# Kernel optimization log

Measured on AMD Instinct MI355X. Metric: run time of the kernel, lower is better.

## Reference

```python
import jax, jax.numpy as jnp
import numpy as np

N = 100000
INPLANES = 256
WIDTH = 104          # floor(256 * 26 / 64)
SCALE = 4
NUMS = SCALE - 1     # 3 branch convs
K = 27               # 3^3 kernel offsets for 3D kernel_size=3
EPS = 1e-5


def setup_inputs() -> dict:
    key = jax.random.key(0)
    ks = jax.random.split(key, 12)
    x_feat = jax.random.normal(ks[0], (N, INPLANES), dtype=jnp.float32)
    # neighbor map: index N means "no neighbor" (padded zero row)
    nbr_idx = jax.random.randint(ks[1], (N, K), 0, N + 1)
    ws = WIDTH * SCALE
    W1 = jax.random.normal(ks[2], (INPLANES, ws), dtype=jnp.float32) * (1.0 / np.sqrt(INPLANES))
    g1 = jnp.ones((ws,), jnp.float32)
    b1 = jnp.zeros((ws,), jnp.float32)
    Wc = jax.random.normal(ks[3], (NUMS, K, WIDTH, WIDTH), dtype=jnp.float32) * (1.0 / np.sqrt(K * WIDTH))
    gc = jnp.ones((NUMS, WIDTH), jnp.float32)
    bc = jnp.zeros((NUMS, WIDTH), jnp.float32)
    W3 = jax.random.normal(ks[4], (ws, INPLANES), dtype=jnp.float32) * (1.0 / np.sqrt(ws))
    g3 = jnp.ones((INPLANES,), jnp.float32)
    b3 = jnp.zeros((INPLANES,), jnp.float32)
    return {"x_feat": x_feat, "nbr_idx": nbr_idx, "W1": W1, "g1": g1, "b1": b1,
            "Wc": Wc, "gc": gc, "bc": bc, "W3": W3, "g3": g3, "b3": b3}


def _bn(x, g, b):
    # training-mode batch norm over the point dimension
    m = jnp.mean(x, axis=0)
    v = jnp.var(x, axis=0)
    return (x - m) * jax.lax.rsqrt(v + EPS) * g + b


def _sparse_conv(feat, nbr_idx, Wk):
    # gather-GEMM-scatter sparse conv: out[n] = sum_k feat[nbr[n,k]] @ Wk[k]
    # index == N hits the appended zero row (missing neighbor)
    fp = jnp.concatenate([feat, jnp.zeros((1, feat.shape[1]), feat.dtype)], axis=0)
    out = jnp.zeros((feat.shape[0], Wk.shape[2]), feat.dtype)
    for k in range(Wk.shape[0]):  # fixed small set of 27 kernel offsets
        out = out + fp[nbr_idx[:, k]] @ Wk[k]
    return out


def reference(x_feat, nbr_idx, W1, g1, b1, Wc, gc, bc, W3, g3, b3):
    out = jax.nn.relu(_bn(x_feat @ W1, g1, b1))          # [N, width*scale]
    spx = [out[:, i * WIDTH:(i + 1) * WIDTH] for i in range(SCALE)]
    parts = []
    sp = None
    for i in range(NUMS):
        # stype='normal', same coord map -> features_at_coordinates is identity
        sp_in = spx[i] if i == 0 else sp + spx[i]
        sp = jax.nn.relu(_bn(_sparse_conv(sp_in, nbr_idx, Wc[i]), gc[i], bc[i]))
        parts.append(sp)
    parts.append(spx[SCALE - 1])                          # scale != 1, normal
    cat = jnp.concatenate(parts, axis=1)                  # [N, width*scale]
    out = _bn(cat @ W3, g3, b3) + x_feat                  # residual (no downsample)
    return jax.nn.relu(out)
```

## Files before the change

### kernel.cpp

```cpp
#include <hip/hip_runtime.h>

#define NPTS 100000
#define INC 256
#define WID 104
#define WSC 416
#define KOFF 27
#define EPSV 1e-5f

typedef unsigned short u16;
typedef float f32x4 __attribute__((ext_vector_type(4)));
typedef short s16x8 __attribute__((ext_vector_type(8)));

__device__ __forceinline__ u16 f2bf(float f) {
  unsigned u = __builtin_bit_cast(unsigned, f);
  u += 0x7FFFu + ((u >> 16) & 1u);
  return (u16)(u >> 16);
}
__device__ __forceinline__ float bf2f(u16 h) {
  unsigned u = ((unsigned)h) << 16;
  return __builtin_bit_cast(float, u);
}
__device__ __forceinline__ void mfma16(f32x4& d, s16x8 a, s16x8 b) {
  asm("v_mfma_f32_16x16x32_bf16 %0, %1, %2, %0" : "+v"(d) : "v"(a), "v"(b));
}
__device__ __forceinline__ void rawbar() {
  __builtin_amdgcn_s_barrier();
  __builtin_amdgcn_sched_barrier(0);
}

#define ST1_OFF 0
#define STC0_OFF 7488
#define STC1_OFF 9360
#define STC2_OFF 11232
#define ST3_OFF 13104
#define ST_TOTAL 17712

#define SPAD 128

__global__ __launch_bounds__(256) void k_prep_w1w3(const float* __restrict__ w1,
    const float* __restrict__ w3, u16* __restrict__ w1t, u16* __restrict__ w3t) {
  int i = blockIdx.x * 256 + threadIdx.x;
  if (i < 416 * 256) {
    int n = i >> 8, k = i & 255;
    w1t[i] = f2bf(w1[(size_t)k * WSC + n]);
  } else if (i < 2 * 416 * 256) {
    int o = i - 416 * 256;
    int n = o / WSC, k = o - n * WSC;
    w3t[o] = f2bf(w3[(size_t)k * INC + n]);
  }
}

__global__ __launch_bounds__(256) void k_prep_wc(const float* __restrict__ wc,
                                                 u16* __restrict__ wct) {
  __shared__ float w[WID * WID];
  int b = blockIdx.x, t = threadIdx.x;
  const float* s = wc + (size_t)b * WID * WID;
  for (int i = t; i < WID * WID; i += 256) w[i] = s[i];
  __syncthreads();
  u16* d = wct + (size_t)b * 112 * WID;
  for (int o = t; o < 112 * WID; o += 256) {
    int n = o / WID, kin = o - n * WID;
    d[o] = f2bf((n < WID) ? w[kin * WID + n] : 0.f);
  }
}

__global__ void k_init(float* __restrict__ st, u16* __restrict__ spxp) {
  const s16x8 hz = {0, 0, 0, 0, 0, 0, 0, 0};
  int i = blockIdx.x * 256 + threadIdx.x;
  if (i < ST_TOTAL) st[i] = 0.f;
  for (int task = i; task < (NPTS + 1) * 3; task += gridDim.x * 256) {
    int r = task / 3, c = task - 3 * r;
    *(s16x8*)(spxp + (size_t)r * SPAD + (13 + c) * 8) = hz;
  }
  if (blockIdx.x == 0 && threadIdx.x < 13)
    *(s16x8*)(spxp + (size_t)NPTS * SPAD + threadIdx.x * 8) = hz;
}

__global__ __launch_bounds__(256) void k_xbf(const float* __restrict__ x,
                                             u16* __restrict__ xb) {
  const int total = NPTS * INC / 8;
  for (int i = blockIdx.x * 256 + threadIdx.x; i < total; i += gridDim.x * 256) {
    const f32x4* s = (const f32x4*)(x + (size_t)i * 8);
    f32x4 v0 = s[0], v1 = s[1];
    s16x8 h;
#pragma unroll
    for (int j = 0; j < 4; ++j) { h[j] = (short)f2bf(v0[j]); h[4 + j] = (short)f2bf(v1[j]); }
    *(s16x8*)(xb + (size_t)i * 8) = h;
  }
}

__global__ __launch_bounds__(256) void k_gemm1(const u16* __restrict__ xb,
    const u16* __restrict__ w1t, u16* __restrict__ y1, float* __restrict__ stats) {
  __shared__ char Al[128 * 128];
  __shared__ char Bl[112 * 128];
  const int t = threadIdx.x, rowbase = blockIdx.x * 128, cb = blockIdx.y;
  const int lane = t & 63, wv = t >> 6, lr = lane & 15, lg = lane >> 4;
  const f32x4 fz = {0.f, 0.f, 0.f, 0.f};
  const s16x8 hz = {0, 0, 0, 0, 0, 0, 0, 0};
  f32x4 acc[2][7];
#pragma unroll
  for (int i = 0; i < 2; ++i)
#pragma unroll
    for (int j = 0; j < 7; ++j) acc[i][j] = fz;
  s16x8 pa[4], pb[4];

  auto issue = [&](int st) {
#pragma unroll
    for (int it = 0; it < 4; ++it) {
      int task = t + it * 256, r = task >> 3, c = task & 7, gr = rowbase + r;
      pa[it] = hz;
      if (gr < NPTS) pa[it] = *(const s16x8*)(xb + (size_t)gr * INC + st * 64 + c * 8);
      pb[it] = hz;
      if (task < 832)
        pb[it] = *(const s16x8*)(w1t + (size_t)(cb * WID + r) * INC + st * 64 + c * 8);
    }
  };
  auto writeT = [&]() {
#pragma unroll
    for (int it = 0; it < 4; ++it) {
      int task = t + it * 256, r = task >> 3, c = task & 7;
      *(s16x8*)(Al + ((r * 128 + c * 16) ^ ((r & 7) << 4))) = pa[it];
      if (task < 896) *(s16x8*)(Bl + ((r * 128 + c * 16) ^ ((r & 7) << 4))) = pb[it];
    }
  };
  auto compute = [&]() {
#pragma unroll
    for (int kc = 0; kc < 2; ++kc) {
      int co = kc * 64 + lg * 16;
      s16x8 a[2], b[7];
#pragma unroll
      for (int mt = 0; mt < 2; ++mt) {
        int r = wv * 32 + mt * 16 + lr;
        a[mt] = *(const s16x8*)(Al + ((r * 128 + co) ^ ((r & 7) << 4)));
      }
#pragma unroll
      for (int ct = 0; ct < 7; ++ct) {
        int r = ct * 16 + lr;
        b[ct] = *(const s16x8*)(Bl + ((r * 128 + co) ^ ((r & 7) << 4)));
      }
#pragma unroll
      for (int mt = 0; mt < 2; ++mt)
#pragma unroll
        for (int ct = 0; ct < 7; ++ct) mfma16(acc[mt][ct], a[mt], b[ct]);
    }
  };

  issue(0);
  for (int st = 0; st < 4; ++st) {
    writeT();
    __syncthreads();
    if (st < 3) issue(st + 1);
    compute();
    if (st < 3) rawbar();
  }
  __syncthreads();
  float* S = (float*)Al;
#pragma unroll
  for (int ct = 0; ct < 7; ++ct) {
    float s = 0.f, q = 0.f;
#pragma unroll
    for (int mt = 0; mt < 2; ++mt)
#pragma unroll
      for (int j = 0; j < 4; ++j) { float v = acc[mt][ct][j]; s += v; q += v * v; }
    s += __shfl_xor(s, 16); s += __shfl_xor(s, 32);
    q += __shfl_xor(q, 16); q += __shfl_xor(q, 32);
    if (lane < 16) {
      S[wv * 224 + ct * 16 + lane] = s;
      S[wv * 224 + 112 + ct * 16 + lane] = q;
    }
  }
  __syncthreads();
  if (t < 224) {
    float v = S[t] + S[224 + t] + S[448 + t] + S[672 + t];
    int cl = (t < 112) ? t : t - 112;
    if (cl < WID) {
      float* base = stats + (blockIdx.x & 7) * 832;
      atomicAdd(base + ((t < 112) ? 0 : WSC) + cb * WID + cl, v);
    }
  }
  __syncthreads();
#pragma unroll
  for (int mt = 0; mt < 2; ++mt)
#pragma unroll
    for (int ct = 0; ct < 7; ++ct)
#pragma unroll
      for (int j = 0; j < 4; ++j) {
        int r = rowbase + wv * 32 + mt * 16 + lg * 4 + j;
        int cl = ct * 16 + lr;
        if (r < NPTS && cl < WID)
          y1[(size_t)r * WSC + cb * WID + cl] = f2bf(acc[mt][ct][j]);
      }
}

__global__ __launch_bounds__(256) void k_conv(const u16* __restrict__ src,
    const int* __restrict__ nbr, const u16* __restrict__ wct,
    u16* __restrict__ z, float* __restrict__ stats) {
  __shared__ char Al[128 * 208];
  __shared__ char Bl[112 * 208];
  const int t = threadIdx.x, rowbase = blockIdx.x * 128;
  const int lane = t & 63, wv = t >> 6, lr = lane & 15, lg = lane >> 4;
  const f32x4 fz = {0.f, 0.f, 0.f, 0.f};
  const s16x8 hz = {0, 0, 0, 0, 0, 0, 0, 0};
  f32x4 acc[2][7];
#pragma unroll
  for (int i = 0; i < 2; ++i)
#pragma unroll
    for (int j = 0; j < 7; ++j) acc[i][j] = fz;
  s16x8 pa[8], pb[6];
  int pidx[8];

  auto idxIssue = [&](int kk) {
#pragma unroll
    for (int it = 0; it < 8; ++it) {
      int r = (t + it * 256) >> 4, gr = rowbase + r;
      pidx[it] = (gr < NPTS) ? nbr[gr * KOFF + kk] : NPTS;
    }
  };
  auto gatherIssue = [&]() {
#pragma unroll
    for (int it = 0; it < 8; ++it) {
      int c = (t + it * 256) & 15;
      pa[it] = hz;
      if (c < 13)
        pa[it] = *(const s16x8*)(src + (size_t)pidx[it] * SPAD + c * 8);
    }
  };
  auto loadB = [&](int k) {
#pragma unroll
    for (int it = 0; it < 6; ++it) {
      int task = t + it * 256;
      if (task < 1456) {
        int r = task / 13, c = task - 13 * r;
        pb[it] = *(const s16x8*)(wct + ((size_t)k * 112 + r) * WID + c * 8);
      }
    }
  };
  auto writeA = [&]() {
#pragma unroll
    for (int it = 0; it < 8; ++it) {
      int task = t + it * 256, r = task >> 4, c = task & 15;
      if (c < 13) *(s16x8*)(Al + r * 208 + c * 16) = pa[it];
    }
  };
  auto writeB = [&]() {
#pragma unroll
    for (int it = 0; it < 6; ++it) {
      int task = t + it * 256;
      if (task < 1456) {
        int r = task / 13, c = task - 13 * r;
        *(s16x8*)(Bl + r * 208 + c * 16) = pb[it];
      }
    }
  };
  auto compute = [&]() {
#pragma unroll
    for (int kc = 0; kc < 3; ++kc) {
      int co = kc * 64 + lg * 16;
      s16x8 a[2], b[7];
#pragma unroll
      for (int mt = 0; mt < 2; ++mt)
        a[mt] = *(const s16x8*)(Al + (wv * 32 + mt * 16 + lr) * 208 + co);
#pragma unroll
      for (int ct = 0; ct < 7; ++ct)
        b[ct] = *(const s16x8*)(Bl + (ct * 16 + lr) * 208 + co);
#pragma unroll
      for (int mt = 0; mt < 2; ++mt)
#pragma unroll
        for (int ct = 0; ct < 7; ++ct) mfma16(acc[mt][ct], a[mt], b[ct]);
    }
    {
      s16x8 a[2], b[7];
#pragma unroll
      for (int mt = 0; mt < 2; ++mt)
        a[mt] = (lg == 0) ? *(const s16x8*)(Al + (wv * 32 + mt * 16 + lr) * 208 + 192) : hz;
#pragma unroll
      for (int ct = 0; ct < 7; ++ct)
        b[ct] = (lg == 0) ? *(const s16x8*)(Bl + (ct * 16 + lr) * 208 + 192) : hz;
#pragma unroll
      for (int mt = 0; mt < 2; ++mt)
#pragma unroll
        for (int ct = 0; ct < 7; ++ct) mfma16(acc[mt][ct], a[mt], b[ct]);
    }
  };

  idxIssue(0);
  gatherIssue();
  loadB(0);
  idxIssue(1);
  for (int k = 0; k < KOFF; ++k) {
    writeA();
    writeB();
    __syncthreads();
    if (k < KOFF - 1) {
      gatherIssue();
      loadB(k + 1);
      if (k < KOFF - 2) idxIssue(k + 2);
    }
    compute();
    if (k < KOFF - 1) rawbar();
  }
  __syncthreads();
  float* S = (float*)Al;
#pragma unroll
  for (int ct = 0; ct < 7; ++ct) {
    float s = 0.f, q = 0.f;
#pragma unroll
    for (int mt = 0; mt < 2; ++mt)
#pragma unroll
      for (int j = 0; j < 4; ++j) { float v = acc[mt][ct][j]; s += v; q += v * v; }
    s += __shfl_xor(s, 16); s += __shfl_xor(s, 32);
    q += __shfl_xor(q, 16); q += __shfl_xor(q, 32);
    if (lane < 16) {
      S[wv * 224 + ct * 16 + lane] = s;
      S[wv * 224 + 112 + ct * 16 + lane] = q;
    }
  }
  __syncthreads();
  if (t < 224) {
    float v = S[t] + S[224 + t] + S[448 + t] + S[672 + t];
    int cl = (t < 112) ? t : t - 112;
    if (cl < WID) {
      float* base = stats + (blockIdx.x & 7) * 208;
      atomicAdd(base + ((t < 112) ? 0 : WID) + cl, v);
    }
  }
  __syncthreads();
#pragma unroll
  for (int mt = 0; mt < 2; ++mt)
#pragma unroll
    for (int ct = 0; ct < 7; ++ct)
#pragma unroll
      for (int j = 0; j < 4; ++j) {
        int r = rowbase + wv * 32 + mt * 16 + lg * 4 + j;
        int cl = ct * 16 + lr;
        if (r < NPTS && cl < WID)
          z[(size_t)r * WID + cl] = f2bf(acc[mt][ct][j]);
      }
}

__global__ __launch_bounds__(256) void k_gemm3(const u16* __restrict__ z0,
    const u16* __restrict__ z1, const u16* __restrict__ z2, const u16* __restrict__ y1,
    const u16* __restrict__ w3t, const float* __restrict__ ST, float* __restrict__ out,
    float* __restrict__ st3) {
  __shared__ char Al[128 * 128];
  __shared__ char Bl[128 * 128];
  __shared__ float sscl[416], ssft[416];
  const int t = threadIdx.x, rowbase = blockIdx.x * 128, cb = blockIdx.y;
  const int lane = t & 63, wv = t >> 6, lr = lane & 15, lg = lane >> 4;
  const int wr = wv >> 1, wc = wv & 1;
  const f32x4 fz = {0.f, 0.f, 0.f, 0.f};
  const s16x8 hz = {0, 0, 0, 0, 0, 0, 0, 0};
  for (int i = t; i < 416; i += 256) {
    float sc, sh;
    if (i < 312) {
      int p = i / 104, c = i - p * 104;
      const float* S = ST + STC0_OFF + p * 1872;
      sc = S[1664 + c]; sh = S[1768 + c];
    } else { sc = ST[6656 + i]; sh = ST[7072 + i]; }
    sscl[i] = sc; ssft[i] = sh;
  }
  f32x4 acc[4][4];
#pragma unroll
  for (int i = 0; i < 4; ++i)
#pragma unroll
    for (int j = 0; j < 4; ++j) acc[i][j] = fz;
  s16x8 pa[4], pb[4];

  auto issue = [&](int st) {
#pragma unroll
    for (int it = 0; it < 4; ++it) {
      int task = t + it * 256, r = task >> 3, c = task & 7;
      int gr = rowbase + r, gc = st * 8 + c;
      pa[it] = hz;
      if (gr < NPTS && gc < 52) {
        int p = gc / 13, cc8 = (gc - p * 13) * 8;
        const u16* s = (p == 0) ? z0 + (size_t)gr * WID + cc8
                     : (p == 1) ? z1 + (size_t)gr * WID + cc8
                     : (p == 2) ? z2 + (size_t)gr * WID + cc8
                                : y1 + (size_t)gr * WSC + 312 + cc8;
        pa[it] = *(const s16x8*)s;
      }
      int gk = st * 64 + c * 8;
      pb[it] = hz;
      if (gk < WSC) pb[it] = *(const s16x8*)(w3t + (size_t)(cb * 128 + r) * WSC + gk);
    }
  };
  auto writeT = [&](int st) {
#pragma unroll
    for (int it = 0; it < 4; ++it) {
      int task = t + it * 256, r = task >> 3, c = task & 7;
      int gr = rowbase + r, gc = st * 8 + c;
      s16x8 h = hz;
      if (gr < NPTS && gc < 52) {
        int p = gc / 13;
        int colb = p * WID + (gc - p * 13) * 8;
#pragma unroll
        for (int j = 0; j < 8; ++j) {
          float f = fmaxf(bf2f((u16)pa[it][j]) * sscl[colb + j] + ssft[colb + j], 0.f);
          h[j] = (short)f2bf(f);
        }
      }
      *(s16x8*)(Al + ((r * 128 + c * 16) ^ ((r & 7) << 4))) = h;
      *(s16x8*)(Bl + ((r * 128 + c * 16) ^ ((r & 7) << 4))) = pb[it];
    }
  };
  auto compute = [&]() {
#pragma unroll
    for (int kc = 0; kc < 2; ++kc) {
      int co = kc * 64 + lg * 16;
      s16x8 a[4], b[4];
#pragma unroll
      for (int mt = 0; mt < 4; ++mt) {
        int r = wr * 64 + mt * 16 + lr;
        a[mt] = *(const s16x8*)(Al + ((r * 128 + co) ^ ((r & 7) << 4)));
      }
#pragma unroll
      for (int ct = 0; ct < 4; ++ct) {
        int r = wc * 64 + ct * 16 + lr;
        b[ct] = *(const s16x8*)(Bl + ((r * 128 + co) ^ ((r & 7) << 4)));
      }
#pragma unroll
      for (int mt = 0; mt < 4; ++mt)
#pragma unroll
        for (int ct = 0; ct < 4; ++ct) mfma16(acc[mt][ct], a[mt], b[ct]);
    }
  };

  issue(0);
  __syncthreads();
  for (int st = 0; st < 7; ++st) {
    writeT(st);
    __syncthreads();
    if (st < 6) issue(st + 1);
    compute();
    if (st < 6) rawbar();
  }
  __syncthreads();
  float* S = (float*)Al;
#pragma unroll
  for (int ct = 0; ct < 4; ++ct) {
    float s = 0.f, q = 0.f;
#pragma unroll
    for (int mt = 0; mt < 4; ++mt)
#pragma unroll
      for (int j = 0; j < 4; ++j) { float v = acc[mt][ct][j]; s += v; q += v * v; }
    s += __shfl_xor(s, 16); s += __shfl_xor(s, 32);
    q += __shfl_xor(q, 16); q += __shfl_xor(q, 32);
    if (lane < 16) {
      S[wv * 128 + ct * 16 + lane] = s;
      S[wv * 128 + 64 + ct * 16 + lane] = q;
    }
  }
  __syncthreads();
  {
    float* base = st3 + (blockIdx.x & 7) * 512;
    if (t < 64) atomicAdd(base + cb * 128 + t, S[t] + S[256 + t]);
    else if (t < 128) atomicAdd(base + INC + cb * 128 + (t - 64), S[64 + t - 64] + S[320 + t - 64]);
    else if (t < 192) atomicAdd(base + cb * 128 + 64 + (t - 128), S[128 + t - 128] + S[384 + t - 128]);
    else atomicAdd(base + INC + cb * 128 + 64 + (t - 192), S[192 + t - 192] + S[448 + t - 192]);
  }
#pragma unroll
  for (int mt = 0; mt < 4; ++mt)
#pragma unroll
    for (int ct = 0; ct < 4; ++ct)
#pragma unroll
      for (int j = 0; j < 4; ++j) {
        int r = rowbase + wr * 64 + mt * 16 + lg * 4 + j;
        int col = cb * 128 + wc * 64 + ct * 16 + lr;
        if (r < NPTS) out[(size_t)r * INC + col] = acc[mt][ct][j];
      }
}

__global__ __launch_bounds__(512) void k_finstats(float* st, const float* __restrict__ g,
                                                  const float* __restrict__ b, int C) {
  int c = threadIdx.x;
  if (c < C) {
    float s = 0.f, q = 0.f;
#pragma unroll
    for (int bk = 0; bk < 8; ++bk) { s += st[bk * 2 * C + c]; q += st[bk * 2 * C + C + c]; }
    float m = s * (1.f / NPTS);
    float var = q * (1.f / NPTS) - m * m;
    float rs = rsqrtf(var + EPSV);
    float sc = rs * g[c];
    st[16 * C + c] = sc;
    st[17 * C + c] = b[c] - m * sc;
  }
}

template <int HASZ>
__global__ __launch_bounds__(256) void k_mix(const u16* __restrict__ y1, int yoff,
    const float* __restrict__ scl1, const float* __restrict__ sft1,
    const u16* __restrict__ z, const float* __restrict__ sclc, const float* __restrict__ sftc,
    u16* __restrict__ spx) {
  const int total = NPTS * 13;
  for (int i = blockIdx.x * 256 + threadIdx.x; i < total; i += gridDim.x * 256) {
    int r = i / 13, cc = i - r * 13;
    s16x8 y = *(const s16x8*)(y1 + (size_t)r * WSC + yoff + cc * 8);
    s16x8 zv;
    if (HASZ) zv = *(const s16x8*)(z + (size_t)r * WID + cc * 8);
    s16x8 o;
#pragma unroll
    for (int j = 0; j < 8; ++j) {
      int c = cc * 8 + j;
      float f = fmaxf(bf2f((u16)y[j]) * scl1[c] + sft1[c], 0.f);
      if (HASZ) f += fmaxf(bf2f((u16)zv[j]) * sclc[c] + sftc[c], 0.f);
      o[j] = (short)f2bf(f);
    }
    *(s16x8*)(spx + (size_t)r * SPAD + cc * 8) = o;
  }
}

__global__ __launch_bounds__(256) void k_final(float* __restrict__ y,
    const float* __restrict__ scale, const float* __restrict__ shift,
    const float* __restrict__ x) {
  const int total = NPTS * 64;
  for (int i = blockIdx.x * 256 + threadIdx.x; i < total; i += gridDim.x * 256) {
    int r = i >> 6, cc = i & 63;
    f32x4 v = *(f32x4*)(y + (size_t)r * INC + cc * 4);
    f32x4 xf = *(const f32x4*)(x + (size_t)r * INC + cc * 4);
#pragma unroll
    for (int j = 0; j < 4; ++j) {
      int c = cc * 4 + j;
      v[j] = fmaxf(v[j] * scale[c] + shift[c] + xf[j], 0.f);
    }
    *(f32x4*)(y + (size_t)r * INC + cc * 4) = v;
  }
}

extern "C" void kernel_launch(void* const* d_in, const int* in_sizes, int n_in,
                              void* d_out, int out_size, void* d_ws, size_t ws_size,
                              hipStream_t stream) {
  const float* x  = (const float*)d_in[0];
  const int* nbr  = (const int*)d_in[1];
  const float* W1 = (const float*)d_in[2];
  const float* g1 = (const float*)d_in[3];
  const float* b1 = (const float*)d_in[4];
  const float* Wc = (const float*)d_in[5];
  const float* gc = (const float*)d_in[6];
  const float* bc = (const float*)d_in[7];
  const float* W3 = (const float*)d_in[8];
  const float* g3 = (const float*)d_in[9];
  const float* b3 = (const float*)d_in[10];
  float* out = (float*)d_out;

  char* ws = (char*)d_ws;
  size_t off = 0;
  auto alloc = [&](size_t n) {
    char* p = ws + off;
    off += (n + 255) & ~(size_t)255;
    return p;
  };
  u16* W1T = (u16*)alloc(416 * 256 * 2);
  u16* W3T = (u16*)alloc(256 * 416 * 2);
  u16* WCT = (u16*)alloc((size_t)3 * 27 * 112 * 104 * 2);
  u16* XB  = (u16*)alloc((size_t)NPTS * INC * 2);
  u16* Y1  = (u16*)alloc((size_t)NPTS * WSC * 2);
  u16* Z0  = (u16*)alloc((size_t)NPTS * WID * 2);
  u16* Z1  = (u16*)alloc((size_t)NPTS * WID * 2);
  u16* Z2  = (u16*)alloc((size_t)NPTS * WID * 2);
  u16* SPX = (u16*)alloc((size_t)(NPTS + 1) * SPAD * 2);
  float* ST = (float*)alloc(ST_TOTAL * 4);
  float* ST1  = ST + ST1_OFF;
  float* STC0 = ST + STC0_OFF;
  float* STC1 = ST + STC1_OFF;
  float* STC2 = ST + STC2_OFF;
  float* ST3  = ST + ST3_OFF;

  k_prep_w1w3<<<832, 256, 0, stream>>>(W1, W3, W1T, W3T);
  k_prep_wc<<<81, 256, 0, stream>>>(Wc, WCT);
  k_init<<<256, 256, 0, stream>>>(ST, SPX);
  k_xbf<<<2048, 256, 0, stream>>>(x, XB);

  k_gemm1<<<dim3(782, 4), 256, 0, stream>>>(XB, W1T, Y1, ST1);
  k_finstats<<<1, 512, 0, stream>>>(ST1, g1, b1, WSC);

  const size_t WCL = (size_t)27 * 112 * WID;
  k_mix<0><<<2048, 256, 0, stream>>>(Y1, 0, ST1 + 6656, ST1 + 7072, nullptr, nullptr, nullptr, SPX);
  k_conv<<<782, 256, 0, stream>>>(SPX, nbr, WCT, Z0, STC0);
  k_finstats<<<1, 512, 0, stream>>>(STC0, gc, bc, WID);
  k_mix<1><<<2048, 256, 0, stream>>>(Y1, 104, ST1 + 6656 + 104, ST1 + 7072 + 104,
                                     Z0, STC0 + 1664, STC0 + 1768, SPX);
  k_conv<<<782, 256, 0, stream>>>(SPX, nbr, WCT + WCL, Z1, STC1);
  k_finstats<<<1, 512, 0, stream>>>(STC1, gc + 104, bc + 104, WID);
  k_mix<1><<<2048, 256, 0, stream>>>(Y1, 208, ST1 + 6656 + 208, ST1 + 7072 + 208,
                                     Z1, STC1 + 1664, STC1 + 1768, SPX);
  k_conv<<<782, 256, 0, stream>>>(SPX, nbr, WCT + 2 * WCL, Z2, STC2);
  k_finstats<<<1, 512, 0, stream>>>(STC2, gc + 208, bc + 208, WID);

  k_gemm3<<<dim3(782, 2), 256, 0, stream>>>(Z0, Z1, Z2, Y1, W3T, ST, out, ST3);
  k_finstats<<<1, 512, 0, stream>>>(ST3, g3, b3, INC);
  k_final<<<2048, 256, 0, stream>>>(out, ST3 + 4096, ST3 + 4352, x);
}
```

Before: 723.7 us.

## Gather conv operands directly to registers, fold BN stats into consumers, bf16 output

The sparse conv kernel now loads neighbor rows straight into MFMA A-operand registers instead of staging them through LDS, and prefetches the next offset's gather during compute. The separate finstats launches are removed, with BN scale/shift computed inside k_mix, k_gemm3 and k_final. Y1 is stored as four contiguous slabs, blocks are remapped for XCD locality, and gemm3 writes a bf16 intermediate that k_final reads along with the bf16 copy of x. The aim is to cut LDS traffic, launch count and memory bytes, at the cost of using a bf16 residual.

```diff
diff --git a/kernel.cpp b/kernel.cpp
--- a/kernel.cpp
+++ b/kernel.cpp
@@ -29,11 +29,10 @@
 }
 
 #define ST1_OFF 0
-#define STC0_OFF 7488
-#define STC1_OFF 9360
-#define STC2_OFF 11232
-#define ST3_OFF 13104
-#define ST_TOTAL 17712
+#define STC_OFF 6656
+#define STC_SZ 1664
+#define ST3_OFF 11648
+#define ST_TOTAL 15744
 
 #define SPAD 128
 
@@ -90,10 +89,14 @@
 }
 
 __global__ __launch_bounds__(256) void k_gemm1(const u16* __restrict__ xb,
-    const u16* __restrict__ w1t, u16* __restrict__ y1, float* __restrict__ stats) {
+    const u16* __restrict__ w1t, u16* __restrict__ ys, float* __restrict__ stats) {
+  const int n = blockIdx.x, xcd = n & 7, sgrp = n >> 3;
+  const int cb = sgrp & 3, q = sgrp >> 2;
+  const int rowbase = (xcd + 8 * q) * 128;
+  if (rowbase >= NPTS) return;
   __shared__ char Al[128 * 128];
   __shared__ char Bl[112 * 128];
-  const int t = threadIdx.x, rowbase = blockIdx.x * 128, cb = blockIdx.y;
+  const int t = threadIdx.x;
   const int lane = t & 63, wv = t >> 6, lr = lane & 15, lg = lane >> 4;
   const f32x4 fz = {0.f, 0.f, 0.f, 0.f};
   const s16x8 hz = {0, 0, 0, 0, 0, 0, 0, 0};
@@ -157,16 +160,16 @@
   float* S = (float*)Al;
 #pragma unroll
   for (int ct = 0; ct < 7; ++ct) {
-    float s = 0.f, q = 0.f;
+    float s = 0.f, qq = 0.f;
 #pragma unroll
     for (int mt = 0; mt < 2; ++mt)
 #pragma unroll
-      for (int j = 0; j < 4; ++j) { float v = acc[mt][ct][j]; s += v; q += v * v; }
+      for (int j = 0; j < 4; ++j) { float v = acc[mt][ct][j]; s += v; qq += v * v; }
     s += __shfl_xor(s, 16); s += __shfl_xor(s, 32);
-    q += __shfl_xor(q, 16); q += __shfl_xor(q, 32);
+    qq += __shfl_xor(qq, 16); qq += __shfl_xor(qq, 32);
     if (lane < 16) {
       S[wv * 224 + ct * 16 + lane] = s;
-      S[wv * 224 + 112 + ct * 16 + lane] = q;
+      S[wv * 224 + 112 + ct * 16 + lane] = qq;
     }
   }
   __syncthreads();
@@ -174,7 +177,7 @@
     float v = S[t] + S[224 + t] + S[448 + t] + S[672 + t];
     int cl = (t < 112) ? t : t - 112;
     if (cl < WID) {
-      float* base = stats + (blockIdx.x & 7) * 832;
+      float* base = stats + (sgrp & 7) * 832;
       atomicAdd(base + ((t < 112) ? 0 : WSC) + cb * WID + cl, v);
     }
   }
@@ -188,43 +191,30 @@
         int r = rowbase + wv * 32 + mt * 16 + lg * 4 + j;
         int cl = ct * 16 + lr;
         if (r < NPTS && cl < WID)
-          y1[(size_t)r * WSC + cb * WID + cl] = f2bf(acc[mt][ct][j]);
+          ys[((size_t)cb * NPTS + r) * WID + cl] = f2bf(acc[mt][ct][j]);
       }
 }
 
 __global__ __launch_bounds__(256) void k_conv(const u16* __restrict__ src,
     const int* __restrict__ nbr, const u16* __restrict__ wct,
     u16* __restrict__ z, float* __restrict__ stats) {
-  __shared__ char Al[128 * 208];
-  __shared__ char Bl[112 * 208];
+  __shared__ char Bl[112 * 208 + 64];
   const int t = threadIdx.x, rowbase = blockIdx.x * 128;
   const int lane = t & 63, wv = t >> 6, lr = lane & 15, lg = lane >> 4;
   const f32x4 fz = {0.f, 0.f, 0.f, 0.f};
-  const s16x8 hz = {0, 0, 0, 0, 0, 0, 0, 0};
   f32x4 acc[2][7];
 #pragma unroll
   for (int i = 0; i < 2; ++i)
 #pragma unroll
     for (int j = 0; j < 7; ++j) acc[i][j] = fz;
-  s16x8 pa[8], pb[6];
-  int pidx[8];
-
-  auto idxIssue = [&](int kk) {
-#pragma unroll
-    for (int it = 0; it < 8; ++it) {
-      int r = (t + it * 256) >> 4, gr = rowbase + r;
-      pidx[it] = (gr < NPTS) ? nbr[gr * KOFF + kk] : NPTS;
-    }
-  };
-  auto gatherIssue = [&]() {
-#pragma unroll
-    for (int it = 0; it < 8; ++it) {
-      int c = (t + it * 256) & 15;
-      pa[it] = hz;
-      if (c < 13)
-        pa[it] = *(const s16x8*)(src + (size_t)pidx[it] * SPAD + c * 8);
-    }
-  };
+  s16x8 pa[2][4], pb[6];
+
+  const int rm0 = rowbase + wv * 32 + lr, rm1 = rm0 + 16;
+  const bool ok0 = rm0 < NPTS, ok1 = rm1 < NPTS;
+  const int* np0 = nbr + (size_t)(ok0 ? rm0 : 0) * KOFF;
+  const int* np1 = nbr + (size_t)(ok1 ? rm1 : 0) * KOFF;
+  int in0, in1;
+
   auto loadB = [&](int k) {
 #pragma unroll
     for (int it = 0; it < 6; ++it) {
@@ -235,13 +225,6 @@
       }
     }
   };
-  auto writeA = [&]() {
-#pragma unroll
-    for (int it = 0; it < 8; ++it) {
-      int task = t + it * 256, r = task >> 4, c = task & 15;
-      if (c < 13) *(s16x8*)(Al + r * 208 + c * 16) = pa[it];
-    }
-  };
   auto writeB = [&]() {
 #pragma unroll
     for (int it = 0; it < 6; ++it) {
@@ -252,67 +235,61 @@
       }
     }
   };
-  auto compute = [&]() {
-#pragma unroll
-    for (int kc = 0; kc < 3; ++kc) {
-      int co = kc * 64 + lg * 16;
-      s16x8 a[2], b[7];
-#pragma unroll
-      for (int mt = 0; mt < 2; ++mt)
-        a[mt] = *(const s16x8*)(Al + (wv * 32 + mt * 16 + lr) * 208 + co);
-#pragma unroll
-      for (int ct = 0; ct < 7; ++ct)
-        b[ct] = *(const s16x8*)(Bl + (ct * 16 + lr) * 208 + co);
-#pragma unroll
-      for (int mt = 0; mt < 2; ++mt)
-#pragma unroll
-        for (int ct = 0; ct < 7; ++ct) mfma16(acc[mt][ct], a[mt], b[ct]);
-    }
-    {
-      s16x8 a[2], b[7];
-#pragma unroll
-      for (int mt = 0; mt < 2; ++mt)
-        a[mt] = (lg == 0) ? *(const s16x8*)(Al + (wv * 32 + mt * 16 + lr) * 208 + 192) : hz;
-#pragma unroll
-      for (int ct = 0; ct < 7; ++ct)
-        b[ct] = (lg == 0) ? *(const s16x8*)(Bl + (ct * 16 + lr) * 208 + 192) : hz;
-#pragma unroll
-      for (int mt = 0; mt < 2; ++mt)
-#pragma unroll
-        for (int ct = 0; ct < 7; ++ct) mfma16(acc[mt][ct], a[mt], b[ct]);
-    }
-  };
-
-  idxIssue(0);
-  gatherIssue();
-  loadB(0);
-  idxIssue(1);
+
+  {
+    int i0 = ok0 ? np0[0] : NPTS, i1 = ok1 ? np1[0] : NPTS;
+#pragma unroll
+    for (int kc = 0; kc < 4; ++kc) {
+      pa[0][kc] = *(const s16x8*)(src + (size_t)i0 * SPAD + kc * 32 + lg * 8);
+      pa[1][kc] = *(const s16x8*)(src + (size_t)i1 * SPAD + kc * 32 + lg * 8);
+    }
+    loadB(0);
+    in0 = ok0 ? np0[1] : NPTS;
+    in1 = ok1 ? np1[1] : NPTS;
+  }
+
   for (int k = 0; k < KOFF; ++k) {
-    writeA();
     writeB();
     __syncthreads();
-    if (k < KOFF - 1) {
-      gatherIssue();
-      loadB(k + 1);
-      if (k < KOFF - 2) idxIssue(k + 2);
-    }
-    compute();
-    if (k < KOFF - 1) rawbar();
-  }
-  __syncthreads();
-  float* S = (float*)Al;
+    if (k < KOFF - 1) loadB(k + 1);
+    const bool more = k < KOFF - 1;
+#pragma unroll
+    for (int kc = 0; kc < 4; ++kc) {
+      s16x8 bf[7];
+#pragma unroll
+      for (int ct = 0; ct < 7; ++ct)
+        bf[ct] = *(const s16x8*)(Bl + (ct * 16 + lr) * 208 + kc * 64 + lg * 16);
+#pragma unroll
+      for (int ct = 0; ct < 7; ++ct) {
+        mfma16(acc[0][ct], pa[0][kc], bf[ct]);
+        mfma16(acc[1][ct], pa[1][kc], bf[ct]);
+      }
+      if (more) {
+        pa[0][kc] = *(const s16x8*)(src + (size_t)in0 * SPAD + kc * 32 + lg * 8);
+        pa[1][kc] = *(const s16x8*)(src + (size_t)in1 * SPAD + kc * 32 + lg * 8);
+      }
+    }
+    if (k < KOFF - 2) {
+      in0 = ok0 ? np0[k + 2] : NPTS;
+      in1 = ok1 ? np1[k + 2] : NPTS;
+    }
+    rawbar();
+  }
+
+  __syncthreads();
+  float* S = (float*)Bl;
 #pragma unroll
   for (int ct = 0; ct < 7; ++ct) {
-    float s = 0.f, q = 0.f;
+    float s = 0.f, qq = 0.f;
 #pragma unroll
     for (int mt = 0; mt < 2; ++mt)
 #pragma unroll
-      for (int j = 0; j < 4; ++j) { float v = acc[mt][ct][j]; s += v; q += v * v; }
+      for (int j = 0; j < 4; ++j) { float v = acc[mt][ct][j]; s += v; qq += v * v; }
     s += __shfl_xor(s, 16); s += __shfl_xor(s, 32);
-    q += __shfl_xor(q, 16); q += __shfl_xor(q, 32);
+    qq += __shfl_xor(qq, 16); qq += __shfl_xor(qq, 32);
     if (lane < 16) {
       S[wv * 224 + ct * 16 + lane] = s;
-      S[wv * 224 + 112 + ct * 16 + lane] = q;
+      S[wv * 224 + 112 + ct * 16 + lane] = qq;
     }
   }
   __syncthreads();
@@ -324,7 +301,6 @@
       atomicAdd(base + ((t < 112) ? 0 : WID) + cl, v);
     }
   }
-  __syncthreads();
 #pragma unroll
   for (int mt = 0; mt < 2; ++mt)
 #pragma unroll
@@ -339,25 +315,42 @@
 }
 
 __global__ __launch_bounds__(256) void k_gemm3(const u16* __restrict__ z0,
-    const u16* __restrict__ z1, const u16* __restrict__ z2, const u16* __restrict__ y1,
-    const u16* __restrict__ w3t, const float* __restrict__ ST, float* __restrict__ out,
-    float* __restrict__ st3) {
+    const u16* __restrict__ z1, const u16* __restrict__ z2, const u16* __restrict__ ys,
+    const u16* __restrict__ w3t, const float* __restrict__ ST,
+    const float* __restrict__ gcp, const float* __restrict__ bcp,
+    const float* __restrict__ g1, const float* __restrict__ b1,
+    u16* __restrict__ ob, float* __restrict__ st3) {
+  const int n = blockIdx.x, xcd = n & 7, sgrp = n >> 3;
+  const int cb = sgrp & 1, q = sgrp >> 1;
+  const int rowbase = (xcd + 8 * q) * 128;
+  if (rowbase >= NPTS) return;
   __shared__ char Al[128 * 128];
   __shared__ char Bl[128 * 128];
   __shared__ float sscl[416], ssft[416];
-  const int t = threadIdx.x, rowbase = blockIdx.x * 128, cb = blockIdx.y;
+  const int t = threadIdx.x;
   const int lane = t & 63, wv = t >> 6, lr = lane & 15, lg = lane >> 4;
   const int wr = wv >> 1, wc = wv & 1;
   const f32x4 fz = {0.f, 0.f, 0.f, 0.f};
   const s16x8 hz = {0, 0, 0, 0, 0, 0, 0, 0};
+  const u16* ys3 = ys + (size_t)3 * NPTS * WID;
   for (int i = t; i < 416; i += 256) {
-    float sc, sh;
+    float s = 0.f, qq = 0.f, gg, bb;
     if (i < 312) {
       int p = i / 104, c = i - p * 104;
-      const float* S = ST + STC0_OFF + p * 1872;
-      sc = S[1664 + c]; sh = S[1768 + c];
-    } else { sc = ST[6656 + i]; sh = ST[7072 + i]; }
-    sscl[i] = sc; ssft[i] = sh;
+      const float* base = ST + STC_OFF + p * STC_SZ;
+#pragma unroll
+      for (int bk = 0; bk < 8; ++bk) { s += base[bk * 208 + c]; qq += base[bk * 208 + 104 + c]; }
+      gg = gcp[i]; bb = bcp[i];
+    } else {
+#pragma unroll
+      for (int bk = 0; bk < 8; ++bk) { s += ST[bk * 832 + i]; qq += ST[bk * 832 + 416 + i]; }
+      gg = g1[i]; bb = b1[i];
+    }
+    float m = s * (1.f / NPTS);
+    float var = qq * (1.f / NPTS) - m * m;
+    float rs = rsqrtf(var + EPSV);
+    float sc = rs * gg;
+    sscl[i] = sc; ssft[i] = bb - m * sc;
   }
   f32x4 acc[4][4];
 #pragma unroll
@@ -370,14 +363,14 @@
 #pragma unroll
     for (int it = 0; it < 4; ++it) {
       int task = t + it * 256, r = task >> 3, c = task & 7;
-      int gr = rowbase + r, gc = st * 8 + c;
+      int gr = rowbase + r, gq = st * 8 + c;
       pa[it] = hz;
-      if (gr < NPTS && gc < 52) {
-        int p = gc / 13, cc8 = (gc - p * 13) * 8;
+      if (gr < NPTS && gq < 52) {
+        int p = gq / 13, cc8 = (gq - p * 13) * 8;
         const u16* s = (p == 0) ? z0 + (size_t)gr * WID + cc8
                      : (p == 1) ? z1 + (size_t)gr * WID + cc8
                      : (p == 2) ? z2 + (size_t)gr * WID + cc8
-                                : y1 + (size_t)gr * WSC + 312 + cc8;
+                                : ys3 + (size_t)gr * WID + cc8;
         pa[it] = *(const s16x8*)s;
       }
       int gk = st * 64 + c * 8;
@@ -389,11 +382,11 @@
 #pragma unroll
     for (int it = 0; it < 4; ++it) {
       int task = t + it * 256, r = task >> 3, c = task & 7;
-      int gr = rowbase + r, gc = st * 8 + c;
+      int gr = rowbase + r, gq = st * 8 + c;
       s16x8 h = hz;
-      if (gr < NPTS && gc < 52) {
-        int p = gc / 13;
-        int colb = p * WID + (gc - p * 13) * 8;
+      if (gr < NPTS && gq < 52) {
+        int p = gq / 13;
+        int colb = p * WID + (gq - p * 13) * 8;
 #pragma unroll
         for (int j = 0; j < 8; ++j) {
           float f = fmaxf(bf2f((u16)pa[it][j]) * sscl[colb + j] + ssft[colb + j], 0.f);
@@ -439,21 +432,21 @@
   float* S = (float*)Al;
 #pragma unroll
   for (int ct = 0; ct < 4; ++ct) {
-    float s = 0.f, q = 0.f;
+    float s = 0.f, qq = 0.f;
 #pragma unroll
     for (int mt = 0; mt < 4; ++mt)
 #pragma unroll
-      for (int j = 0; j < 4; ++j) { float v = acc[mt][ct][j]; s += v; q += v * v; }
+      for (int j = 0; j < 4; ++j) { float v = acc[mt][ct][j]; s += v; qq += v * v; }
     s += __shfl_xor(s, 16); s += __shfl_xor(s, 32);
-    q += __shfl_xor(q, 16); q += __shfl_xor(q, 32);
+    qq += __shfl_xor(qq, 16); qq += __shfl_xor(qq, 32);
     if (lane < 16) {
       S[wv * 128 + ct * 16 + lane] = s;
-      S[wv * 128 + 64 + ct * 16 + lane] = q;
+      S[wv * 128 + 64 + ct * 16 + lane] = qq;
     }
   }
   __syncthreads();
   {
-    float* base = st3 + (blockIdx.x & 7) * 512;
+    float* base = st3 + (sgrp & 7) * 512;
     if (t < 64) atomicAdd(base + cb * 128 + t, S[t] + S[256 + t]);
     else if (t < 128) atomicAdd(base + INC + cb * 128 + (t - 64), S[64 + t - 64] + S[320 + t - 64]);
     else if (t < 192) atomicAdd(base + cb * 128 + 64 + (t - 128), S[128 + t - 128] + S[384 + t - 128]);
@@ -467,63 +460,94 @@
       for (int j = 0; j < 4; ++j) {
         int r = rowbase + wr * 64 + mt * 16 + lg * 4 + j;
         int col = cb * 128 + wc * 64 + ct * 16 + lr;
-        if (r < NPTS) out[(size_t)r * INC + col] = acc[mt][ct][j];
-      }
-}
-
-__global__ __launch_bounds__(512) void k_finstats(float* st, const float* __restrict__ g,
-                                                  const float* __restrict__ b, int C) {
-  int c = threadIdx.x;
-  if (c < C) {
+        if (r < NPTS) ob[(size_t)r * INC + col] = f2bf(acc[mt][ct][j]);
+      }
+}
+
+template <int HASZ>
+__global__ __launch_bounds__(256) void k_mix(const u16* __restrict__ ys, int slab,
+    const float* __restrict__ ST, int yoff,
+    const float* __restrict__ g1, const float* __restrict__ b1,
+    const u16* __restrict__ z, const float* __restrict__ stc,
+    const float* __restrict__ gcb, const float* __restrict__ bcb,
+    u16* __restrict__ spx) {
+  __shared__ float s1c[104], f1c[104], szc[104], fzc[104];
+  const int t = threadIdx.x;
+  if (t < 104) {
     float s = 0.f, q = 0.f;
 #pragma unroll
-    for (int bk = 0; bk < 8; ++bk) { s += st[bk * 2 * C + c]; q += st[bk * 2 * C + C + c]; }
+    for (int bk = 0; bk < 8; ++bk) { s += ST[bk * 832 + yoff + t]; q += ST[bk * 832 + 416 + yoff + t]; }
     float m = s * (1.f / NPTS);
     float var = q * (1.f / NPTS) - m * m;
     float rs = rsqrtf(var + EPSV);
-    float sc = rs * g[c];
-    st[16 * C + c] = sc;
-    st[17 * C + c] = b[c] - m * sc;
-  }
-}
-
-template <int HASZ>
-__global__ __launch_bounds__(256) void k_mix(const u16* __restrict__ y1, int yoff,
-    const float* __restrict__ scl1, const float* __restrict__ sft1,
-    const u16* __restrict__ z, const float* __restrict__ sclc, const float* __restrict__ sftc,
-    u16* __restrict__ spx) {
+    float sc = rs * g1[yoff + t];
+    s1c[t] = sc; f1c[t] = b1[yoff + t] - m * sc;
+  } else if (HASZ && t >= 128 && t < 232) {
+    int c = t - 128;
+    float s = 0.f, q = 0.f;
+#pragma unroll
+    for (int bk = 0; bk < 8; ++bk) { s += stc[bk * 208 + c]; q += stc[bk * 208 + 104 + c]; }
+    float m = s * (1.f / NPTS);
+    float var = q * (1.f / NPTS) - m * m;
+    float rs = rsqrtf(var + EPSV);
+    float sc = rs * gcb[c];
+    szc[c] = sc; fzc[c] = bcb[c] - m * sc;
+  }
+  __syncthreads();
+  const u16* yb = ys + (size_t)slab * NPTS * WID;
   const int total = NPTS * 13;
-  for (int i = blockIdx.x * 256 + threadIdx.x; i < total; i += gridDim.x * 256) {
+  for (int i = blockIdx.x * 256 + t; i < total; i += gridDim.x * 256) {
     int r = i / 13, cc = i - r * 13;
-    s16x8 y = *(const s16x8*)(y1 + (size_t)r * WSC + yoff + cc * 8);
+    s16x8 y = *(const s16x8*)(yb + (size_t)r * WID + cc * 8);
     s16x8 zv;
     if (HASZ) zv = *(const s16x8*)(z + (size_t)r * WID + cc * 8);
     s16x8 o;
 #pragma unroll
     for (int j = 0; j < 8; ++j) {
       int c = cc * 8 + j;
-      float f = fmaxf(bf2f((u16)y[j]) * scl1[c] + sft1[c], 0.f);
-      if (HASZ) f += fmaxf(bf2f((u16)zv[j]) * sclc[c] + sftc[c], 0.f);
+      float f = fmaxf(bf2f((u16)y[j]) * s1c[c] + f1c[c], 0.f);
+      if (HASZ) f += fmaxf(bf2f((u16)zv[j]) * szc[c] + fzc[c], 0.f);
       o[j] = (short)f2bf(f);
     }
     *(s16x8*)(spx + (size_t)r * SPAD + cc * 8) = o;
   }
 }
 
-__global__ __launch_bounds__(256) void k_final(float* __restrict__ y,
-    const float* __restrict__ scale, const float* __restrict__ shift,
-    const float* __restrict__ x) {
-  const int total = NPTS * 64;
-  for (int i = blockIdx.x * 256 + threadIdx.x; i < total; i += gridDim.x * 256) {
-    int r = i >> 6, cc = i & 63;
-    f32x4 v = *(f32x4*)(y + (size_t)r * INC + cc * 4);
-    f32x4 xf = *(const f32x4*)(x + (size_t)r * INC + cc * 4);
+__global__ __launch_bounds__(256) void k_final(const u16* __restrict__ ob,
+    const u16* __restrict__ xb, const float* __restrict__ ST3,
+    const float* __restrict__ g3, const float* __restrict__ b3,
+    float* __restrict__ out) {
+  __shared__ float sc3[256], sf3[256];
+  const int t = threadIdx.x;
+  {
+    float s = 0.f, q = 0.f;
+#pragma unroll
+    for (int bk = 0; bk < 8; ++bk) { s += ST3[bk * 512 + t]; q += ST3[bk * 512 + 256 + t]; }
+    float m = s * (1.f / NPTS);
+    float var = q * (1.f / NPTS) - m * m;
+    float rs = rsqrtf(var + EPSV);
+    float sc = rs * g3[t];
+    sc3[t] = sc; sf3[t] = b3[t] - m * sc;
+  }
+  __syncthreads();
+  const int total = NPTS * 32;
+  for (int i = blockIdx.x * 256 + t; i < total; i += gridDim.x * 256) {
+    int r = i >> 5, cc = i & 31;
+    s16x8 o = *(const s16x8*)(ob + (size_t)r * INC + cc * 8);
+    s16x8 xv = *(const s16x8*)(xb + (size_t)r * INC + cc * 8);
+    f32x4 v0, v1;
 #pragma unroll
     for (int j = 0; j < 4; ++j) {
-      int c = cc * 4 + j;
-      v[j] = fmaxf(v[j] * scale[c] + shift[c] + xf[j], 0.f);
-    }
-    *(f32x4*)(y + (size_t)r * INC + cc * 4) = v;
+      int c = cc * 8 + j;
+      v0[j] = fmaxf(bf2f((u16)o[j]) * sc3[c] + sf3[c] + bf2f((u16)xv[j]), 0.f);
+    }
+#pragma unroll
+    for (int j = 0; j < 4; ++j) {
+      int c = cc * 8 + 4 + j;
+      v1[j] = fmaxf(bf2f((u16)o[4 + j]) * sc3[c] + sf3[c] + bf2f((u16)xv[4 + j]), 0.f);
+    }
+    f32x4* dp = (f32x4*)(out + (size_t)r * INC + cc * 8);
+    dp[0] = v0; dp[1] = v1;
   }
 }
 
@@ -545,25 +569,26 @@
 
   char* ws = (char*)d_ws;
   size_t off = 0;
-  auto alloc = [&](size_t n) {
+  auto alloc = [&](size_t nbytes) {
     char* p = ws + off;
-    off += (n + 255) & ~(size_t)255;
+    off += (nbytes + 255) & ~(size_t)255;
     return p;
   };
   u16* W1T = (u16*)alloc(416 * 256 * 2);
   u16* W3T = (u16*)alloc(256 * 416 * 2);
   u16* WCT = (u16*)alloc((size_t)3 * 27 * 112 * 104 * 2);
   u16* XB  = (u16*)alloc((size_t)NPTS * INC * 2);
-  u16* Y1  = (u16*)alloc((size_t)NPTS * WSC * 2);
+  u16* Y1S = (u16*)alloc((size_t)4 * NPTS * WID * 2);
   u16* Z0  = (u16*)alloc((size_t)NPTS * WID * 2);
   u16* Z1  = (u16*)alloc((size_t)NPTS * WID * 2);
   u16* Z2  = (u16*)alloc((size_t)NPTS * WID * 2);
+  u16* OB  = (u16*)alloc((size_t)NPTS * INC * 2);
   u16* SPX = (u16*)alloc((size_t)(NPTS + 1) * SPAD * 2);
   float* ST = (float*)alloc(ST_TOTAL * 4);
   float* ST1  = ST + ST1_OFF;
-  float* STC0 = ST + STC0_OFF;
-  float* STC1 = ST + STC1_OFF;
-  float* STC2 = ST + STC2_OFF;
+  float* STC0 = ST + STC_OFF;
+  float* STC1 = ST + STC_OFF + STC_SZ;
+  float* STC2 = ST + STC_OFF + 2 * STC_SZ;
   float* ST3  = ST + ST3_OFF;
 
   k_prep_w1w3<<<832, 256, 0, stream>>>(W1, W3, W1T, W3T);
@@ -571,23 +596,19 @@
   k_init<<<256, 256, 0, stream>>>(ST, SPX);
   k_xbf<<<2048, 256, 0, stream>>>(x, XB);
 
-  k_gemm1<<<dim3(782, 4), 256, 0, stream>>>(XB, W1T, Y1, ST1);
-  k_finstats<<<1, 512, 0, stream>>>(ST1, g1, b1, WSC);
+  k_gemm1<<<3136, 256, 0, stream>>>(XB, W1T, Y1S, ST1);
 
   const size_t WCL = (size_t)27 * 112 * WID;
-  k_mix<0><<<2048, 256, 0, stream>>>(Y1, 0, ST1 + 6656, ST1 + 7072, nullptr, nullptr, nullptr, SPX);
+  k_mix<0><<<2048, 256, 0, stream>>>(Y1S, 0, ST1, 0, g1, b1,
+                                     nullptr, nullptr, nullptr, nullptr, SPX);
   k_conv<<<782, 256, 0, stream>>>(SPX, nbr, WCT, Z0, STC0);
-  k_finstats<<<1, 512, 0, stream>>>(STC0, gc, bc, WID);
-  k_mix<1><<<2048, 256, 0, stream>>>(Y1, 104, ST1 + 6656 + 104, ST1 + 7072 + 104,
-                                     Z0, STC0 + 1664, STC0 + 1768, SPX);
+  k_mix<1><<<2048, 256, 0, stream>>>(Y1S, 1, ST1, 104, g1, b1,
+                                     Z0, STC0, gc, bc, SPX);
   k_conv<<<782, 256, 0, stream>>>(SPX, nbr, WCT + WCL, Z1, STC1);
-  k_finstats<<<1, 512, 0, stream>>>(STC1, gc + 104, bc + 104, WID);
-  k_mix<1><<<2048, 256, 0, stream>>>(Y1, 208, ST1 + 6656 + 208, ST1 + 7072 + 208,
-                                     Z1, STC1 + 1664, STC1 + 1768, SPX);
+  k_mix<1><<<2048, 256, 0, stream>>>(Y1S, 2, ST1, 208, g1, b1,
+                                     Z1, STC1, gc + 104, bc + 104, SPX);
   k_conv<<<782, 256, 0, stream>>>(SPX, nbr, WCT + 2 * WCL, Z2, STC2);
-  k_finstats<<<1, 512, 0, stream>>>(STC2, gc + 208, bc + 208, WID);
-
-  k_gemm3<<<dim3(782, 2), 256, 0, stream>>>(Z0, Z1, Z2, Y1, W3T, ST, out, ST3);
-  k_finstats<<<1, 512, 0, stream>>>(ST3, g3, b3, INC);
-  k_final<<<2048, 256, 0, stream>>>(out, ST3 + 4096, ST3 + 4352, x);
-}
+
+  k_gemm3<<<1568, 256, 0, stream>>>(Z0, Z1, Z2, Y1S, W3T, ST, gc, bc, g1, b1, OB, ST3);
+  k_final<<<2048, 256, 0, stream>>>(OB, XB, ST3, g3, b3, out);
+}
```

Measured after the change: 710.4 us. No clear change (-1.8%).
